# Kernel optimization log

Measured on AMD Instinct MI355X. Metric: run time of the kernel, lower is better.

Reference implementation:

```python
import jax, jax.numpy as jnp
import numpy as np

N_NODES = 50000
N_EDGES = 800000
D_IN = 96
D_OUT = 96


def setup_inputs() -> dict:
    key = jax.random.key(0)
    k1, k2, k3, k4 = jax.random.split(key, 4)
    feat = jax.random.normal(k1, (N_NODES, D_IN), dtype=jnp.float32)
    # xavier_normal-like init for weight, zeros bias (as in the torch module)
    std = (2.0 / (D_IN + D_OUT)) ** 0.5
    weight = jax.random.normal(k2, (D_IN, D_OUT), dtype=jnp.float32) * std
    bias = jnp.zeros((D_OUT,), dtype=jnp.float32)
    src = jax.random.randint(k3, (N_EDGES,), 0, N_NODES, dtype=jnp.int64)
    dst = jax.random.randint(k4, (N_EDGES,), 0, N_NODES, dtype=jnp.int64)
    return {"feat": feat, "weight": weight, "bias": bias, "src": src, "dst": dst}


def reference(feat, weight, bias, src, dst):
    N = feat.shape[0]
    ones = jnp.ones(src.shape[0], dtype=feat.dtype)
    out_deg = jax.ops.segment_sum(ones, src, num_segments=N)  # out-degree per node
    in_deg = jax.ops.segment_sum(ones, dst, num_segments=N)   # in-degree per node
    ci = jnp.clip(out_deg, 1.0, None) ** -0.5                 # src-side norm
    cj = jnp.clip(in_deg, 1.0, None) ** -0.5                  # dst-side norm
    # gather src features * ci, scatter-sum to dst, scale by cj
    msg = feat[src] * ci[src, None]                           # [E, D_IN]
    agg = jax.ops.segment_sum(msg, dst, num_segments=N) * cj[:, None]
    # DGL UDF reduce only updates nodes that receive messages; isolated
    # (zero in-degree) nodes keep their original features.
    h = jnp.where(in_deg[:, None] > 0, agg, feat)
    return jnp.matmul(h, weight) + bias
```

## Files before the change

### kernel.cpp

```cpp
#include <hip/hip_runtime.h>

#define N_NODES 50000
#define N_EDGES 800000
#define D 96
#define D4 (D / 4)

#define RL 12
#define HPAD 13

#define NB 196
#define ECAP 5120
#define SCAP 5120
#define HCCAP 3072
#define PA_BLOCKS 400
#define PA_CHUNK 2000
#define SB_BLOCKS 392
#define WPREP_TB 5

typedef __attribute__((ext_vector_type(8))) short short8;
typedef __attribute__((ext_vector_type(4))) float floatx4;

__device__ __forceinline__ short8 as_short8(uint4 u) { return *(short8*)&u; }

__device__ __forceinline__ unsigned bf16pack(float a, float b) {
    unsigned ua = __float_as_uint(a);
    unsigned ub = __float_as_uint(b);
    ua = (ua + 0x7FFFu + ((ua >> 16) & 1u)) >> 16;
    ub = (ub + 0x7FFFu + ((ub >> 16) & 1u)) & 0xFFFF0000u;
    return ua | ub;
}

__global__ void __launch_bounds__(1024) sortA_kernel(
        const int* __restrict__ src, const int* __restrict__ dst,
        unsigned* __restrict__ gcur,
        unsigned* __restrict__ ebuf, unsigned short* __restrict__ sbuf) {
    __shared__ unsigned raw[PA_CHUNK];
    __shared__ unsigned ord[PA_CHUNK];
    __shared__ unsigned short sord[PA_CHUNK];
    __shared__ unsigned hist[512];
    __shared__ unsigned sc[512], lstart[512], cur[512], gbase[512];
    int t = threadIdx.x;
    int e0 = blockIdx.x * PA_CHUNK;
    if (t < 512) hist[t] = 0;
    __syncthreads();
    for (int i = t; i < PA_CHUNK; i += 1024) {
        int s = src[e0 + i];
        int d = dst[e0 + i];
        raw[i] = ((unsigned)d << 16) | (unsigned)s;
        atomicAdd(&hist[d >> 8], 1u);
        atomicAdd(&hist[256 + (s >> 8)], 1u);
    }
    __syncthreads();
    if (t < 512) sc[t] = hist[t];
    __syncthreads();
    for (int o = 1; o < 256; o <<= 1) {
        unsigned v = 0;
        if (t < 512 && (t & 255) >= o) v = sc[t - o];
        __syncthreads();
        if (t < 512 && (t & 255) >= o) sc[t] += v;
        __syncthreads();
    }
    if (t < 512) {
        unsigned ls = sc[t] - hist[t];
        lstart[t] = ls;
        cur[t] = ls;
        if ((t & 255) < NB)
            gbase[t] = atomicAdd(&gcur[(t >> 8) * NB + (t & 255)], hist[t]);
    }
    __syncthreads();
    for (int i = t; i < PA_CHUNK; i += 1024) {
        unsigned r = raw[i];
        unsigned p = atomicAdd(&cur[r >> 24], 1u);
        ord[p] = r;
        unsigned s = r & 0xFFFFu;
        unsigned q = atomicAdd(&cur[256 + (s >> 8)], 1u);
        sord[q] = (unsigned short)s;
    }
    __syncthreads();
    for (int i = t; i < PA_CHUNK; i += 1024) {
        unsigned r = ord[i];
        unsigned bd = r >> 24;
        unsigned pos = gbase[bd] + ((unsigned)i - lstart[bd]);
        if (pos < ECAP) ebuf[bd * ECAP + pos] = r;
        unsigned s = sord[i];
        unsigned bs = 256 + (s >> 8);
        unsigned pos2 = gbase[bs] + ((unsigned)i - lstart[bs]);
        if (pos2 < SCAP) sbuf[(size_t)(bs - 256) * SCAP + pos2] = (unsigned short)s;
    }
}

__global__ void __launch_bounds__(1024) sortB_kernel(
        const unsigned* __restrict__ gcur, const unsigned* __restrict__ ebuf,
        const unsigned short* __restrict__ sbuf,
        const float4* __restrict__ feat4, const float* __restrict__ W,
        unsigned* __restrict__ WT32,
        int* __restrict__ deg_in, int* __restrict__ off,
        unsigned short* __restrict__ csr, uint4* __restrict__ sfeat) {
    int blk = blockIdx.x;
    if (blk >= SB_BLOCKS) {
        int t = (blk - SB_BLOCKS) * 1024 + threadIdx.x;
        if (t >= D * (D / 2)) return;
        int n = t / (D / 2);
        int j = t - n * (D / 2);
        float w0 = W[(2 * j) * D + n];
        float w1 = W[(2 * j + 1) * D + n];
        WT32[n * (D / 2) + j] = bf16pack(w0, w1);
        return;
    }
    __shared__ unsigned short csr_l[HCCAP];
    __shared__ unsigned dcount[128], dcur[128], scount[128];
    __shared__ unsigned wtot, tot_s;
    int b = blk >> 1;
    unsigned half = (unsigned)(blk & 1);
    int t = threadIdx.x;
    unsigned cntd = gcur[b];      if (cntd > ECAP) cntd = ECAP;
    unsigned cnts = gcur[NB + b]; if (cnts > SCAP) cnts = SCAP;
    if (t < 128) { dcount[t] = 0; scount[t] = 0; }
    __syncthreads();
    const unsigned* __restrict__ sg = ebuf + (size_t)b * ECAP;
    for (int i = t; i < (int)cntd; i += 1024) {
        unsigned loc = (sg[i] >> 16) & 255u;
        if ((loc >> 7) == half) atomicAdd(&dcount[loc & 127u], 1u);
    }
    const unsigned short* __restrict__ ss = sbuf + (size_t)b * SCAP;
    for (int i = t; i < (int)cnts; i += 1024) {
        unsigned loc = ss[i] & 255u;
        if ((loc >> 7) == half) atomicAdd(&scount[loc & 127u], 1u);
    }
    __syncthreads();
    unsigned pad = 0, incl = 0;
    if (t < 128) {
        pad = (dcount[t] + 7u) & ~7u;
        incl = pad;
        int lane = t & 63;
#pragma unroll
        for (int st = 1; st < 64; st <<= 1) {
            unsigned u = __shfl_up(incl, st, 64);
            if (lane >= st) incl += u;
        }
        if (t == 63) wtot = incl;
    }
    __syncthreads();
    if (t < 128) {
        if (t >= 64) incl += wtot;
        unsigned ex = incl - pad;
        dcur[t] = ex;
        if (t == 127) tot_s = incl;
        int n = b * 256 + (int)(half << 7) + t;
        if (n < N_NODES) {
            deg_in[n] = (int)dcount[t];
            off[n] = blk * HCCAP + (int)ex;
        }
    }
    __syncthreads();
    for (int i = t; i < (int)cntd; i += 1024) {
        unsigned r = sg[i];
        unsigned loc = (r >> 16) & 255u;
        if ((loc >> 7) == half) {
            unsigned p = atomicAdd(&dcur[loc & 127u], 1u);
            if (p < HCCAP) csr_l[p] = (unsigned short)(r & 0xFFFFu);
        }
    }
    __syncthreads();
    unsigned tot = tot_s;
    if (tot > HCCAP) tot = HCCAP;
    unsigned* __restrict__ og = (unsigned*)(csr + (size_t)blk * HCCAP);
    const unsigned* __restrict__ cl = (const unsigned*)csr_l;
    for (int i = t; i < (int)(tot >> 1); i += 1024) og[i] = cl[i];
    int base_n = b * 256 + (int)(half << 7);
    for (int r = t; r < 128 * RL; r += 1024) {
        int nl = r / RL;
        int lane = r - nl * RL;
        int n = base_n + nl;
        if (n < N_NODES) {
            float c = rsqrtf(fmaxf((float)scount[nl], 1.0f));
            float4 a = feat4[(size_t)n * D4 + lane * 2];
            float4 bb = feat4[(size_t)n * D4 + lane * 2 + 1];
            uint4 o;
            o.x = bf16pack(a.x * c, a.y * c);
            o.y = bf16pack(a.z * c, a.w * c);
            o.z = bf16pack(bb.x * c, bb.y * c);
            o.w = bf16pack(bb.z * c, bb.w * c);
            sfeat[(size_t)n * RL + lane] = o;
        }
    }
}

__global__ void __launch_bounds__(192) gather_mm_kernel(
        const float4* __restrict__ feat4, const uint4* __restrict__ sfeat,
        const int* __restrict__ deg_in, const int* __restrict__ off,
        const unsigned short* __restrict__ csr, const uint4* __restrict__ wt4,
        const float* __restrict__ bias, float* __restrict__ out) {
    __shared__ uint4 sh[16 * HPAD];
    int tid = threadIdx.x;
    {
        int g = tid / RL;
        int lane = tid - g * RL;
        int n = blockIdx.x * 16 + g;
        int deg = deg_in[n];
        uint4* __restrict__ hout = &sh[g * HPAD + lane];
        if (deg == 0) {
            float4 a = feat4[n * D4 + lane * 2];
            float4 b = feat4[n * D4 + lane * 2 + 1];
            uint4 o;
            o.x = bf16pack(a.x, a.y);
            o.y = bf16pack(a.z, a.w);
            o.z = bf16pack(b.x, b.y);
            o.w = bf16pack(b.z, b.w);
            *hout = o;
        } else {
            const unsigned short* __restrict__ bk = csr + off[n];
            const uint4* __restrict__ sf = sfeat + lane;
            float acc[8] = {};
#define ACC8(v)  { \
        acc[0] += __uint_as_float((v).x << 16); \
        acc[1] += __uint_as_float((v).x & 0xFFFF0000u); \
        acc[2] += __uint_as_float((v).y << 16); \
        acc[3] += __uint_as_float((v).y & 0xFFFF0000u); \
        acc[4] += __uint_as_float((v).z << 16); \
        acc[5] += __uint_as_float((v).z & 0xFFFF0000u); \
        acc[6] += __uint_as_float((v).w << 16); \
        acc[7] += __uint_as_float((v).w & 0xFFFF0000u); }
            int i = 0;
            int full16 = deg & ~15;
            for (; i < full16; i += 16) {
                uint4 ia = *(const uint4*)(bk + i);
                uint4 ib = *(const uint4*)(bk + i + 8);
                unsigned s0 = ia.x & 0xFFFFu, s1 = ia.x >> 16;
                unsigned s2 = ia.y & 0xFFFFu, s3 = ia.y >> 16;
                unsigned s4 = ia.z & 0xFFFFu, s5 = ia.z >> 16;
                unsigned s6 = ia.w & 0xFFFFu, s7 = ia.w >> 16;
                unsigned s8 = ib.x & 0xFFFFu, s9 = ib.x >> 16;
                unsigned sa = ib.y & 0xFFFFu, sb = ib.y >> 16;
                unsigned sx = ib.z & 0xFFFFu, sd = ib.z >> 16;
                unsigned se = ib.w & 0xFFFFu, sfi = ib.w >> 16;
                uint4 v0 = sf[(size_t)s0 * RL];
                uint4 v1 = sf[(size_t)s1 * RL];
                uint4 v2 = sf[(size_t)s2 * RL];
                uint4 v3 = sf[(size_t)s3 * RL];
                uint4 v4 = sf[(size_t)s4 * RL];
                uint4 v5 = sf[(size_t)s5 * RL];
                uint4 v6 = sf[(size_t)s6 * RL];
                uint4 v7 = sf[(size_t)s7 * RL];
                uint4 v8 = sf[(size_t)s8 * RL];
                uint4 v9 = sf[(size_t)s9 * RL];
                uint4 va = sf[(size_t)sa * RL];
                uint4 vb = sf[(size_t)sb * RL];
                uint4 vc = sf[(size_t)sx * RL];
                uint4 vd = sf[(size_t)sd * RL];
                uint4 ve = sf[(size_t)se * RL];
                uint4 vf = sf[(size_t)sfi * RL];
                ACC8(v0); ACC8(v1); ACC8(v2); ACC8(v3);
                ACC8(v4); ACC8(v5); ACC8(v6); ACC8(v7);
                ACC8(v8); ACC8(v9); ACC8(va); ACC8(vb);
                ACC8(vc); ACC8(vd); ACC8(ve); ACC8(vf);
            }
            int full8 = deg & ~7;
            for (; i < full8; i += 8) {
                uint4 idx = *(const uint4*)(bk + i);
                unsigned s0 = idx.x & 0xFFFFu, s1 = idx.x >> 16;
                unsigned s2 = idx.y & 0xFFFFu, s3 = idx.y >> 16;
                unsigned s4 = idx.z & 0xFFFFu, s5 = idx.z >> 16;
                unsigned s6 = idx.w & 0xFFFFu, s7 = idx.w >> 16;
                uint4 v0 = sf[(size_t)s0 * RL];
                uint4 v1 = sf[(size_t)s1 * RL];
                uint4 v2 = sf[(size_t)s2 * RL];
                uint4 v3 = sf[(size_t)s3 * RL];
                uint4 v4 = sf[(size_t)s4 * RL];
                uint4 v5 = sf[(size_t)s5 * RL];
                uint4 v6 = sf[(size_t)s6 * RL];
                uint4 v7 = sf[(size_t)s7 * RL];
                ACC8(v0); ACC8(v1); ACC8(v2); ACC8(v3);
                ACC8(v4); ACC8(v5); ACC8(v6); ACC8(v7);
            }
            for (; i < deg; ++i) {
                uint4 v = sf[(size_t)bk[i] * RL];
                ACC8(v);
            }
#undef ACC8
            float cj = rsqrtf((float)deg);
            uint4 o;
            o.x = bf16pack(acc[0] * cj, acc[1] * cj);
            o.y = bf16pack(acc[2] * cj, acc[3] * cj);
            o.z = bf16pack(acc[4] * cj, acc[5] * cj);
            o.w = bf16pack(acc[6] * cj, acc[7] * cj);
            *hout = o;
        }
    }
    __syncthreads();
    int wave = tid >> 6;
    int lane = tid & 63;
    int m = lane & 15, quad = lane >> 4;
    short8 a0 = as_short8(sh[m * HPAD + quad]);
    short8 a1 = as_short8(sh[m * HPAD + 4 + quad]);
    short8 a2 = as_short8(sh[m * HPAD + 8 + quad]);
    int row0 = blockIdx.x * 16;
    int r_out0 = row0 + quad * 4;
#pragma unroll
    for (int ct = wave * 2; ct < wave * 2 + 2; ++ct) {
        int n = ct * 16 + m;
        int wb = n * RL + quad;
        short8 b0 = as_short8(wt4[wb]);
        short8 b1 = as_short8(wt4[wb + 4]);
        short8 b2 = as_short8(wt4[wb + 8]);
        floatx4 c = {0.f, 0.f, 0.f, 0.f};
        c = __builtin_amdgcn_mfma_f32_16x16x32_bf16(a0, b0, c, 0, 0, 0);
        c = __builtin_amdgcn_mfma_f32_16x16x32_bf16(a1, b1, c, 0, 0, 0);
        c = __builtin_amdgcn_mfma_f32_16x16x32_bf16(a2, b2, c, 0, 0, 0);
        float bs = bias[n];
#pragma unroll
        for (int r = 0; r < 4; ++r)
            out[(size_t)(r_out0 + r) * D + n] = c[r] + bs;
    }
}

extern "C" void kernel_launch(void* const* d_in, const int* in_sizes, int n_in,
                              void* d_out, int out_size, void* d_ws, size_t ws_size,
                              hipStream_t stream) {
    const float* feat = (const float*)d_in[0];
    const float* W    = (const float*)d_in[1];
    const float* bias = (const float*)d_in[2];
    const int*   src  = (const int*)d_in[3];
    const int*   dst  = (const int*)d_in[4];

    unsigned*       gcur    = (unsigned*)d_ws;
    int*            deg_in  = (int*)(gcur + 2 * NB);
    int*            off     = deg_in + N_NODES;
    unsigned*       ebuf    = (unsigned*)(off + N_NODES);
    unsigned short* sbuf    = (unsigned short*)(ebuf + (size_t)NB * ECAP);
    unsigned short* csr     = sbuf + (size_t)NB * SCAP;
    uint4*          sfeat   = (uint4*)(csr + (size_t)SB_BLOCKS * HCCAP);
    unsigned*       WT32    = (unsigned*)(sfeat + (size_t)N_NODES * RL);

    hipMemsetAsync(gcur, 0, 2 * NB * sizeof(unsigned), stream);
    sortA_kernel<<<PA_BLOCKS, 1024, 0, stream>>>(src, dst, gcur, ebuf, sbuf);
    sortB_kernel<<<SB_BLOCKS + WPREP_TB, 1024, 0, stream>>>(
        gcur, ebuf, sbuf, (const float4*)feat, W, WT32, deg_in, off, csr, sfeat);
    gather_mm_kernel<<<N_NODES / 16, 192, 0, stream>>>(
        (const float4*)feat, sfeat, deg_in, off, csr, (const uint4*)WT32,
        bias, (float*)d_out);
}
```

Before: 139.8 us.

## Split neighbor gather across two thread teams and merge sortB halves

The gather kernel now runs 384 threads per 16-node tile. Two teams of 192 threads each take alternating 8-edge chunks of each node's neighbor list, and the partial sums are combined through shared memory before the MFMA transform. Each of the six waves then computes one 16-column output tile instead of two. sortB goes back to one block per 256-node bucket, staging the edge bucket in shared memory so the global buffer is read once instead of twice, at the cost of larger LDS use and fewer blocks. The aim is more memory-level parallelism for the latency-bound gather, in exchange for an extra shared-memory reduction and a barrier.

```diff
diff --git a/kernel.cpp b/kernel.cpp
--- a/kernel.cpp
+++ b/kernel.cpp
@@ -11,10 +11,9 @@
 #define NB 196
 #define ECAP 5120
 #define SCAP 5120
-#define HCCAP 3072
+#define CCAP 6144
 #define PA_BLOCKS 400
 #define PA_CHUNK 2000
-#define SB_BLOCKS 392
 #define WPREP_TB 5
 
 typedef __attribute__((ext_vector_type(8))) short short8;
@@ -97,39 +96,38 @@
         int* __restrict__ deg_in, int* __restrict__ off,
         unsigned short* __restrict__ csr, uint4* __restrict__ sfeat) {
     int blk = blockIdx.x;
-    if (blk >= SB_BLOCKS) {
-        int t = (blk - SB_BLOCKS) * 1024 + threadIdx.x;
-        if (t >= D * (D / 2)) return;
-        int n = t / (D / 2);
-        int j = t - n * (D / 2);
+    if (blk >= NB) {
+        int t2 = (blk - NB) * 1024 + threadIdx.x;
+        if (t2 >= D * (D / 2)) return;
+        int n = t2 / (D / 2);
+        int j = t2 - n * (D / 2);
         float w0 = W[(2 * j) * D + n];
         float w1 = W[(2 * j + 1) * D + n];
         WT32[n * (D / 2) + j] = bf16pack(w0, w1);
         return;
     }
-    __shared__ unsigned short csr_l[HCCAP];
-    __shared__ unsigned dcount[128], dcur[128], scount[128];
-    __shared__ unsigned wtot, tot_s;
-    int b = blk >> 1;
-    unsigned half = (unsigned)(blk & 1);
+    __shared__ unsigned eb[ECAP];
+    __shared__ unsigned short csr_l[CCAP];
+    __shared__ unsigned dcount[256], dcur[256], scount[256], wsum[4];
+    __shared__ unsigned tot_s;
+    int b = blk;
     int t = threadIdx.x;
     unsigned cntd = gcur[b];      if (cntd > ECAP) cntd = ECAP;
     unsigned cnts = gcur[NB + b]; if (cnts > SCAP) cnts = SCAP;
-    if (t < 128) { dcount[t] = 0; scount[t] = 0; }
+    if (t < 256) { dcount[t] = 0; scount[t] = 0; }
     __syncthreads();
     const unsigned* __restrict__ sg = ebuf + (size_t)b * ECAP;
     for (int i = t; i < (int)cntd; i += 1024) {
-        unsigned loc = (sg[i] >> 16) & 255u;
-        if ((loc >> 7) == half) atomicAdd(&dcount[loc & 127u], 1u);
+        unsigned r = sg[i];
+        eb[i] = r;
+        atomicAdd(&dcount[(r >> 16) & 255u], 1u);
     }
     const unsigned short* __restrict__ ss = sbuf + (size_t)b * SCAP;
-    for (int i = t; i < (int)cnts; i += 1024) {
-        unsigned loc = ss[i] & 255u;
-        if ((loc >> 7) == half) atomicAdd(&scount[loc & 127u], 1u);
-    }
+    for (int i = t; i < (int)cnts; i += 1024)
+        atomicAdd(&scount[ss[i] & 255u], 1u);
     __syncthreads();
     unsigned pad = 0, incl = 0;
-    if (t < 128) {
+    if (t < 256) {
         pad = (dcount[t] + 7u) & ~7u;
         incl = pad;
         int lane = t & 63;
@@ -138,40 +136,39 @@
             unsigned u = __shfl_up(incl, st, 64);
             if (lane >= st) incl += u;
         }
-        if (t == 63) wtot = incl;
-    }
-    __syncthreads();
-    if (t < 128) {
-        if (t >= 64) incl += wtot;
+        if (lane == 63) wsum[t >> 6] = incl;
+    }
+    __syncthreads();
+    if (t < 256) {
+        int w = t >> 6;
+        unsigned base = 0;
+        for (int k = 0; k < w; ++k) base += wsum[k];
+        incl += base;
         unsigned ex = incl - pad;
         dcur[t] = ex;
-        if (t == 127) tot_s = incl;
-        int n = b * 256 + (int)(half << 7) + t;
+        if (t == 255) tot_s = incl;
+        int n = b * 256 + t;
         if (n < N_NODES) {
             deg_in[n] = (int)dcount[t];
-            off[n] = blk * HCCAP + (int)ex;
+            off[n] = b * CCAP + (int)ex;
         }
     }
     __syncthreads();
     for (int i = t; i < (int)cntd; i += 1024) {
-        unsigned r = sg[i];
-        unsigned loc = (r >> 16) & 255u;
-        if ((loc >> 7) == half) {
-            unsigned p = atomicAdd(&dcur[loc & 127u], 1u);
-            if (p < HCCAP) csr_l[p] = (unsigned short)(r & 0xFFFFu);
-        }
+        unsigned r = eb[i];
+        unsigned p = atomicAdd(&dcur[(r >> 16) & 255u], 1u);
+        if (p < CCAP) csr_l[p] = (unsigned short)(r & 0xFFFFu);
     }
     __syncthreads();
     unsigned tot = tot_s;
-    if (tot > HCCAP) tot = HCCAP;
-    unsigned* __restrict__ og = (unsigned*)(csr + (size_t)blk * HCCAP);
+    if (tot > CCAP) tot = CCAP;
+    unsigned* __restrict__ og = (unsigned*)(csr + (size_t)b * CCAP);
     const unsigned* __restrict__ cl = (const unsigned*)csr_l;
     for (int i = t; i < (int)(tot >> 1); i += 1024) og[i] = cl[i];
-    int base_n = b * 256 + (int)(half << 7);
-    for (int r = t; r < 128 * RL; r += 1024) {
-        int nl = r / RL;
-        int lane = r - nl * RL;
-        int n = base_n + nl;
+    for (int r2 = t; r2 < 256 * RL; r2 += 1024) {
+        int nl = r2 / RL;
+        int lane = r2 - nl * RL;
+        int n = b * 256 + nl;
         if (n < N_NODES) {
             float c = rsqrtf(fmaxf((float)scount[nl], 1.0f));
             float4 a = feat4[(size_t)n * D4 + lane * 2];
@@ -186,32 +183,31 @@
     }
 }
 
-__global__ void __launch_bounds__(192) gather_mm_kernel(
+__global__ void __launch_bounds__(384) gather_mm_kernel(
         const float4* __restrict__ feat4, const uint4* __restrict__ sfeat,
         const int* __restrict__ deg_in, const int* __restrict__ off,
         const unsigned short* __restrict__ csr, const uint4* __restrict__ wt4,
         const float* __restrict__ bias, float* __restrict__ out) {
+    __shared__ float shp[16][D];
     __shared__ uint4 sh[16 * HPAD];
     int tid = threadIdx.x;
-    {
-        int g = tid / RL;
-        int lane = tid - g * RL;
-        int n = blockIdx.x * 16 + g;
-        int deg = deg_in[n];
-        uint4* __restrict__ hout = &sh[g * HPAD + lane];
-        if (deg == 0) {
-            float4 a = feat4[n * D4 + lane * 2];
-            float4 b = feat4[n * D4 + lane * 2 + 1];
-            uint4 o;
-            o.x = bf16pack(a.x, a.y);
-            o.y = bf16pack(a.z, a.w);
-            o.z = bf16pack(b.x, b.y);
-            o.w = bf16pack(b.z, b.w);
-            *hout = o;
-        } else {
-            const unsigned short* __restrict__ bk = csr + off[n];
-            const uint4* __restrict__ sf = sfeat + lane;
-            float acc[8] = {};
+    int team = (tid >= 192) ? 1 : 0;
+    int r = tid - team * 192;
+    int g = r / RL;
+    int lane = r - g * RL;
+    int n = blockIdx.x * 16 + g;
+    int deg = deg_in[n];
+    float acc[8] = {};
+    if (deg == 0) {
+        if (team == 0) {
+            float4 a = feat4[(size_t)n * D4 + lane * 2];
+            float4 b = feat4[(size_t)n * D4 + lane * 2 + 1];
+            acc[0] = a.x; acc[1] = a.y; acc[2] = a.z; acc[3] = a.w;
+            acc[4] = b.x; acc[5] = b.y; acc[6] = b.z; acc[7] = b.w;
+        }
+    } else {
+        const unsigned short* __restrict__ bk = csr + off[n];
+        const uint4* __restrict__ sf = sfeat + lane;
 #define ACC8(v)  { \
         acc[0] += __uint_as_float((v).x << 16); \
         acc[1] += __uint_as_float((v).x & 0xFFFF0000u); \
@@ -221,97 +217,75 @@
         acc[5] += __uint_as_float((v).z & 0xFFFF0000u); \
         acc[6] += __uint_as_float((v).w << 16); \
         acc[7] += __uint_as_float((v).w & 0xFFFF0000u); }
-            int i = 0;
-            int full16 = deg & ~15;
-            for (; i < full16; i += 16) {
-                uint4 ia = *(const uint4*)(bk + i);
-                uint4 ib = *(const uint4*)(bk + i + 8);
-                unsigned s0 = ia.x & 0xFFFFu, s1 = ia.x >> 16;
-                unsigned s2 = ia.y & 0xFFFFu, s3 = ia.y >> 16;
-                unsigned s4 = ia.z & 0xFFFFu, s5 = ia.z >> 16;
-                unsigned s6 = ia.w & 0xFFFFu, s7 = ia.w >> 16;
-                unsigned s8 = ib.x & 0xFFFFu, s9 = ib.x >> 16;
-                unsigned sa = ib.y & 0xFFFFu, sb = ib.y >> 16;
-                unsigned sx = ib.z & 0xFFFFu, sd = ib.z >> 16;
-                unsigned se = ib.w & 0xFFFFu, sfi = ib.w >> 16;
-                uint4 v0 = sf[(size_t)s0 * RL];
-                uint4 v1 = sf[(size_t)s1 * RL];
-                uint4 v2 = sf[(size_t)s2 * RL];
-                uint4 v3 = sf[(size_t)s3 * RL];
-                uint4 v4 = sf[(size_t)s4 * RL];
-                uint4 v5 = sf[(size_t)s5 * RL];
-                uint4 v6 = sf[(size_t)s6 * RL];
-                uint4 v7 = sf[(size_t)s7 * RL];
-                uint4 v8 = sf[(size_t)s8 * RL];
-                uint4 v9 = sf[(size_t)s9 * RL];
-                uint4 va = sf[(size_t)sa * RL];
-                uint4 vb = sf[(size_t)sb * RL];
-                uint4 vc = sf[(size_t)sx * RL];
-                uint4 vd = sf[(size_t)sd * RL];
-                uint4 ve = sf[(size_t)se * RL];
-                uint4 vf = sf[(size_t)sfi * RL];
-                ACC8(v0); ACC8(v1); ACC8(v2); ACC8(v3);
-                ACC8(v4); ACC8(v5); ACC8(v6); ACC8(v7);
-                ACC8(v8); ACC8(v9); ACC8(va); ACC8(vb);
-                ACC8(vc); ACC8(vd); ACC8(ve); ACC8(vf);
-            }
-            int full8 = deg & ~7;
-            for (; i < full8; i += 8) {
-                uint4 idx = *(const uint4*)(bk + i);
-                unsigned s0 = idx.x & 0xFFFFu, s1 = idx.x >> 16;
-                unsigned s2 = idx.y & 0xFFFFu, s3 = idx.y >> 16;
-                unsigned s4 = idx.z & 0xFFFFu, s5 = idx.z >> 16;
-                unsigned s6 = idx.w & 0xFFFFu, s7 = idx.w >> 16;
-                uint4 v0 = sf[(size_t)s0 * RL];
-                uint4 v1 = sf[(size_t)s1 * RL];
-                uint4 v2 = sf[(size_t)s2 * RL];
-                uint4 v3 = sf[(size_t)s3 * RL];
-                uint4 v4 = sf[(size_t)s4 * RL];
-                uint4 v5 = sf[(size_t)s5 * RL];
-                uint4 v6 = sf[(size_t)s6 * RL];
-                uint4 v7 = sf[(size_t)s7 * RL];
-                ACC8(v0); ACC8(v1); ACC8(v2); ACC8(v3);
-                ACC8(v4); ACC8(v5); ACC8(v6); ACC8(v7);
-            }
-            for (; i < deg; ++i) {
-                uint4 v = sf[(size_t)bk[i] * RL];
+        for (int i = team * 8; i + 8 <= deg; i += 16) {
+            uint4 idx = *(const uint4*)(bk + i);
+            unsigned s0 = idx.x & 0xFFFFu, s1 = idx.x >> 16;
+            unsigned s2 = idx.y & 0xFFFFu, s3 = idx.y >> 16;
+            unsigned s4 = idx.z & 0xFFFFu, s5 = idx.z >> 16;
+            unsigned s6 = idx.w & 0xFFFFu, s7 = idx.w >> 16;
+            uint4 v0 = sf[(size_t)s0 * RL];
+            uint4 v1 = sf[(size_t)s1 * RL];
+            uint4 v2 = sf[(size_t)s2 * RL];
+            uint4 v3 = sf[(size_t)s3 * RL];
+            uint4 v4 = sf[(size_t)s4 * RL];
+            uint4 v5 = sf[(size_t)s5 * RL];
+            uint4 v6 = sf[(size_t)s6 * RL];
+            uint4 v7 = sf[(size_t)s7 * RL];
+            ACC8(v0); ACC8(v1); ACC8(v2); ACC8(v3);
+            ACC8(v4); ACC8(v5); ACC8(v6); ACC8(v7);
+        }
+        int ts = deg & ~7;
+        if (((ts >> 3) & 1) == team) {
+            for (int j = ts; j < deg; ++j) {
+                uint4 v = sf[(size_t)bk[j] * RL];
                 ACC8(v);
             }
+        }
 #undef ACC8
-            float cj = rsqrtf((float)deg);
-            uint4 o;
-            o.x = bf16pack(acc[0] * cj, acc[1] * cj);
-            o.y = bf16pack(acc[2] * cj, acc[3] * cj);
-            o.z = bf16pack(acc[4] * cj, acc[5] * cj);
-            o.w = bf16pack(acc[6] * cj, acc[7] * cj);
-            *hout = o;
-        }
+    }
+    if (team == 0) {
+#pragma unroll
+        for (int j = 0; j < 8; ++j) shp[g][lane * 8 + j] = acc[j];
+    }
+    __syncthreads();
+    if (team == 1) {
+        float cj = (deg > 0) ? rsqrtf((float)deg) : 1.0f;
+        float s0 = (shp[g][lane * 8 + 0] + acc[0]) * cj;
+        float s1 = (shp[g][lane * 8 + 1] + acc[1]) * cj;
+        float s2 = (shp[g][lane * 8 + 2] + acc[2]) * cj;
+        float s3 = (shp[g][lane * 8 + 3] + acc[3]) * cj;
+        float s4 = (shp[g][lane * 8 + 4] + acc[4]) * cj;
+        float s5 = (shp[g][lane * 8 + 5] + acc[5]) * cj;
+        float s6 = (shp[g][lane * 8 + 6] + acc[6]) * cj;
+        float s7 = (shp[g][lane * 8 + 7] + acc[7]) * cj;
+        uint4 o;
+        o.x = bf16pack(s0, s1);
+        o.y = bf16pack(s2, s3);
+        o.z = bf16pack(s4, s5);
+        o.w = bf16pack(s6, s7);
+        sh[g * HPAD + lane] = o;
     }
     __syncthreads();
     int wave = tid >> 6;
-    int lane = tid & 63;
-    int m = lane & 15, quad = lane >> 4;
+    int lane64 = tid & 63;
+    int m = lane64 & 15, quad = lane64 >> 4;
     short8 a0 = as_short8(sh[m * HPAD + quad]);
     short8 a1 = as_short8(sh[m * HPAD + 4 + quad]);
     short8 a2 = as_short8(sh[m * HPAD + 8 + quad]);
-    int row0 = blockIdx.x * 16;
-    int r_out0 = row0 + quad * 4;
+    int nn = wave * 16 + m;
+    int wb = nn * RL + quad;
+    short8 b0 = as_short8(wt4[wb]);
+    short8 b1 = as_short8(wt4[wb + 4]);
+    short8 b2 = as_short8(wt4[wb + 8]);
+    floatx4 c = {0.f, 0.f, 0.f, 0.f};
+    c = __builtin_amdgcn_mfma_f32_16x16x32_bf16(a0, b0, c, 0, 0, 0);
+    c = __builtin_amdgcn_mfma_f32_16x16x32_bf16(a1, b1, c, 0, 0, 0);
+    c = __builtin_amdgcn_mfma_f32_16x16x32_bf16(a2, b2, c, 0, 0, 0);
+    float bs = bias[nn];
+    int r_out0 = blockIdx.x * 16 + quad * 4;
 #pragma unroll
-    for (int ct = wave * 2; ct < wave * 2 + 2; ++ct) {
-        int n = ct * 16 + m;
-        int wb = n * RL + quad;
-        short8 b0 = as_short8(wt4[wb]);
-        short8 b1 = as_short8(wt4[wb + 4]);
-        short8 b2 = as_short8(wt4[wb + 8]);
-        floatx4 c = {0.f, 0.f, 0.f, 0.f};
-        c = __builtin_amdgcn_mfma_f32_16x16x32_bf16(a0, b0, c, 0, 0, 0);
-        c = __builtin_amdgcn_mfma_f32_16x16x32_bf16(a1, b1, c, 0, 0, 0);
-        c = __builtin_amdgcn_mfma_f32_16x16x32_bf16(a2, b2, c, 0, 0, 0);
-        float bs = bias[n];
-#pragma unroll
-        for (int r = 0; r < 4; ++r)
-            out[(size_t)(r_out0 + r) * D + n] = c[r] + bs;
-    }
+    for (int rr = 0; rr < 4; ++rr)
+        out[(size_t)(r_out0 + rr) * D + nn] = c[rr] + bs;
 }
 
 extern "C" void kernel_launch(void* const* d_in, const int* in_sizes, int n_in,
@@ -329,14 +303,14 @@
     unsigned*       ebuf    = (unsigned*)(off + N_NODES);
     unsigned short* sbuf    = (unsigned short*)(ebuf + (size_t)NB * ECAP);
     unsigned short* csr     = sbuf + (size_t)NB * SCAP;
-    uint4*          sfeat   = (uint4*)(csr + (size_t)SB_BLOCKS * HCCAP);
+    uint4*          sfeat   = (uint4*)(csr + (size_t)NB * CCAP);
     unsigned*       WT32    = (unsigned*)(sfeat + (size_t)N_NODES * RL);
 
     hipMemsetAsync(gcur, 0, 2 * NB * sizeof(unsigned), stream);
     sortA_kernel<<<PA_BLOCKS, 1024, 0, stream>>>(src, dst, gcur, ebuf, sbuf);
-    sortB_kernel<<<SB_BLOCKS + WPREP_TB, 1024, 0, stream>>>(
+    sortB_kernel<<<NB + WPREP_TB, 1024, 0, stream>>>(
         gcur, ebuf, sbuf, (const float4*)feat, W, WT32, deg_in, off, csr, sfeat);
-    gather_mm_kernel<<<N_NODES / 16, 192, 0, stream>>>(
+    gather_mm_kernel<<<N_NODES / 16, 384, 0, stream>>>(
         (const float4*)feat, sfeat, deg_in, off, csr, (const uint4*)WT32,
         bias, (float*)d_out);
 }
```

Result: no change. 140.9 us (+0.8%).

## Fuse sort, CSR build and gather-matmul into one cooperative persistent kernel

Applied to the files above, without the earlier changes.

Merges the three kernel launches into a single cooperative kernel of 256 blocks that uses grid-wide syncs between phases: edge bucketing, per-bucket CSR/degree construction (one block per 256-node bucket instead of two half-buckets), and the gather plus MFMA matmul. The last phase loops over tiles, with five 192-thread groups per block. This removes launch gaps and the duplicated ebuf/sbuf scans. In exchange it runs with only 256 blocks, so latency hiding in the gather phase is lower, and it adds the cost of the grid syncs.

```diff
diff --git a/kernel.cpp b/kernel.cpp
--- a/kernel.cpp
+++ b/kernel.cpp
@@ -1,4 +1,7 @@
 #include <hip/hip_runtime.h>
+#include <hip/hip_cooperative_groups.h>
+
+namespace cg = cooperative_groups;
 
 #define N_NODES 50000
 #define N_EDGES 800000
@@ -11,11 +14,10 @@
 #define NB 196
 #define ECAP 5120
 #define SCAP 5120
-#define HCCAP 3072
-#define PA_BLOCKS 400
-#define PA_CHUNK 2000
-#define SB_BLOCKS 392
-#define WPREP_TB 5
+#define CCAP 6144
+#define PA_CHUNK 3125
+#define GRID_BLKS 256
+#define NT 3125
 
 typedef __attribute__((ext_vector_type(8))) short short8;
 typedef __attribute__((ext_vector_type(4))) float floatx4;
@@ -30,188 +32,207 @@
     return ua | ub;
 }
 
-__global__ void __launch_bounds__(1024) sortA_kernel(
+__global__ void __launch_bounds__(1024) fused_kernel(
         const int* __restrict__ src, const int* __restrict__ dst,
-        unsigned* __restrict__ gcur,
-        unsigned* __restrict__ ebuf, unsigned short* __restrict__ sbuf) {
-    __shared__ unsigned raw[PA_CHUNK];
-    __shared__ unsigned ord[PA_CHUNK];
-    __shared__ unsigned short sord[PA_CHUNK];
-    __shared__ unsigned hist[512];
-    __shared__ unsigned sc[512], lstart[512], cur[512], gbase[512];
+        const float4* __restrict__ feat4, const float* __restrict__ W,
+        const float* __restrict__ bias,
+        unsigned* __restrict__ gcur, unsigned* __restrict__ ebuf,
+        unsigned short* __restrict__ sbuf, unsigned short* __restrict__ csr,
+        uint4* __restrict__ sfeat, unsigned* __restrict__ WT32,
+        int* __restrict__ deg_in, int* __restrict__ off,
+        float* __restrict__ out) {
+    __shared__ __align__(16) char smem[41600];
+    __shared__ unsigned wsum8[8];
+    __shared__ unsigned tot_s;
+    cg::grid_group grid = cg::this_grid();
     int t = threadIdx.x;
-    int e0 = blockIdx.x * PA_CHUNK;
-    if (t < 512) hist[t] = 0;
-    __syncthreads();
-    for (int i = t; i < PA_CHUNK; i += 1024) {
-        int s = src[e0 + i];
-        int d = dst[e0 + i];
-        raw[i] = ((unsigned)d << 16) | (unsigned)s;
-        atomicAdd(&hist[d >> 8], 1u);
-        atomicAdd(&hist[256 + (s >> 8)], 1u);
+    int blk = blockIdx.x;
+
+    {
+        unsigned*       raw    = (unsigned*)(smem);
+        unsigned*       ord    = (unsigned*)(smem + 12544);
+        unsigned short* sord   = (unsigned short*)(smem + 25088);
+        unsigned*       hist   = (unsigned*)(smem + 31360);
+        unsigned*       lstart = (unsigned*)(smem + 35456);
+        unsigned*       cur    = (unsigned*)(smem + 37504);
+        unsigned*       gbase  = (unsigned*)(smem + 39552);
+        int e0 = blk * PA_CHUNK;
+        if (t < 512) hist[t] = 0;
+        __syncthreads();
+        for (int i = t; i < PA_CHUNK; i += 1024) {
+            int s = src[e0 + i];
+            int d = dst[e0 + i];
+            raw[i] = ((unsigned)d << 16) | (unsigned)s;
+            atomicAdd(&hist[d >> 8], 1u);
+            atomicAdd(&hist[256 + (s >> 8)], 1u);
+        }
+        __syncthreads();
+        unsigned h = 0, incl = 0;
+        if (t < 512) {
+            h = hist[t];
+            incl = h;
+            int lane = t & 63;
+#pragma unroll
+            for (int st = 1; st < 64; st <<= 1) {
+                unsigned u = __shfl_up(incl, st, 64);
+                if (lane >= st) incl += u;
+            }
+            if (lane == 63) wsum8[t >> 6] = incl;
+        }
+        __syncthreads();
+        if (t < 512) {
+            int w = t >> 6;
+            int h0 = (t >> 8) * 4;
+            unsigned base = 0;
+            for (int k = h0; k < w; ++k) base += wsum8[k];
+            incl += base;
+            unsigned ls = incl - h;
+            lstart[t] = ls;
+            cur[t] = ls;
+            if ((t & 255) < NB)
+                gbase[t] = atomicAdd(&gcur[(t >> 8) * NB + (t & 255)], h);
+        }
+        __syncthreads();
+        for (int i = t; i < PA_CHUNK; i += 1024) {
+            unsigned r = raw[i];
+            unsigned p = atomicAdd(&cur[r >> 24], 1u);
+            ord[p] = r;
+            unsigned s = r & 0xFFFFu;
+            unsigned q = atomicAdd(&cur[256 + (s >> 8)], 1u);
+            sord[q] = (unsigned short)s;
+        }
+        __syncthreads();
+        for (int i = t; i < PA_CHUNK; i += 1024) {
+            unsigned r = ord[i];
+            unsigned bd = r >> 24;
+            unsigned pos = gbase[bd] + ((unsigned)i - lstart[bd]);
+            if (pos < ECAP) ebuf[bd * ECAP + pos] = r;
+            unsigned s = sord[i];
+            unsigned bs = 256 + (s >> 8);
+            unsigned pos2 = gbase[bs] + ((unsigned)i - lstart[bs]);
+            if (pos2 < SCAP) sbuf[(size_t)(bs - 256) * SCAP + pos2] = (unsigned short)s;
+        }
     }
-    __syncthreads();
-    if (t < 512) sc[t] = hist[t];
-    __syncthreads();
-    for (int o = 1; o < 256; o <<= 1) {
-        unsigned v = 0;
-        if (t < 512 && (t & 255) >= o) v = sc[t - o];
-        __syncthreads();
-        if (t < 512 && (t & 255) >= o) sc[t] += v;
-        __syncthreads();
+    __threadfence();
+    grid.sync();
+
+    if (blk < NB) {
+        unsigned*       eb     = (unsigned*)(smem);
+        unsigned short* csr_l  = (unsigned short*)(smem + 20480);
+        unsigned*       dcount = (unsigned*)(smem + 32768);
+        unsigned*       dcur   = (unsigned*)(smem + 33792);
+        unsigned*       scount = (unsigned*)(smem + 34816);
+        int b = blk;
+        unsigned cntd = gcur[b];      if (cntd > ECAP) cntd = ECAP;
+        unsigned cnts = gcur[NB + b]; if (cnts > SCAP) cnts = SCAP;
+        if (t < 256) { dcount[t] = 0; scount[t] = 0; }
+        __syncthreads();
+        const unsigned* __restrict__ sg = ebuf + (size_t)b * ECAP;
+        for (int i = t; i < (int)cntd; i += 1024) {
+            unsigned r = sg[i];
+            eb[i] = r;
+            atomicAdd(&dcount[(r >> 16) & 255u], 1u);
+        }
+        const unsigned short* __restrict__ ss = sbuf + (size_t)b * SCAP;
+        for (int i = t; i < (int)cnts; i += 1024)
+            atomicAdd(&scount[ss[i] & 255u], 1u);
+        __syncthreads();
+        unsigned pad = 0, incl = 0;
+        if (t < 256) {
+            pad = (dcount[t] + 7u) & ~7u;
+            incl = pad;
+            int lane = t & 63;
+#pragma unroll
+            for (int st = 1; st < 64; st <<= 1) {
+                unsigned u = __shfl_up(incl, st, 64);
+                if (lane >= st) incl += u;
+            }
+            if (lane == 63) wsum8[t >> 6] = incl;
+        }
+        __syncthreads();
+        if (t < 256) {
+            int w = t >> 6;
+            unsigned base = 0;
+            for (int k = 0; k < w; ++k) base += wsum8[k];
+            incl += base;
+            unsigned ex = incl - pad;
+            dcur[t] = ex;
+            if (t == 255) tot_s = incl;
+            int n = b * 256 + t;
+            if (n < N_NODES) {
+                deg_in[n] = (int)dcount[t];
+                off[n] = b * CCAP + (int)ex;
+            }
+        }
+        __syncthreads();
+        for (int i = t; i < (int)cntd; i += 1024) {
+            unsigned r = eb[i];
+            unsigned p = atomicAdd(&dcur[(r >> 16) & 255u], 1u);
+            if (p < CCAP) csr_l[p] = (unsigned short)(r & 0xFFFFu);
+        }
+        __syncthreads();
+        unsigned tot = tot_s;
+        if (tot > CCAP) tot = CCAP;
+        unsigned* __restrict__ og = (unsigned*)(csr + (size_t)b * CCAP);
+        const unsigned* __restrict__ cl = (const unsigned*)csr_l;
+        for (int i = t; i < (int)(tot >> 1); i += 1024) og[i] = cl[i];
+        for (int r2 = t; r2 < 256 * RL; r2 += 1024) {
+            int nl = r2 / RL;
+            int lane = r2 - nl * RL;
+            int n = b * 256 + nl;
+            if (n < N_NODES) {
+                float c = rsqrtf(fmaxf((float)scount[nl], 1.0f));
+                float4 a = feat4[(size_t)n * D4 + lane * 2];
+                float4 bb = feat4[(size_t)n * D4 + lane * 2 + 1];
+                uint4 o;
+                o.x = bf16pack(a.x * c, a.y * c);
+                o.y = bf16pack(a.z * c, a.w * c);
+                o.z = bf16pack(bb.x * c, bb.y * c);
+                o.w = bf16pack(bb.z * c, bb.w * c);
+                sfeat[(size_t)n * RL + lane] = o;
+            }
+        }
+    } else {
+        int t2 = (blk - NB) * 1024 + t;
+        if (t2 < D * (D / 2)) {
+            int n = t2 / (D / 2);
+            int j = t2 - n * (D / 2);
+            float w0 = W[(2 * j) * D + n];
+            float w1 = W[(2 * j + 1) * D + n];
+            WT32[n * (D / 2) + j] = bf16pack(w0, w1);
+        }
     }
-    if (t < 512) {
-        unsigned ls = sc[t] - hist[t];
-        lstart[t] = ls;
-        cur[t] = ls;
-        if ((t & 255) < NB)
-            gbase[t] = atomicAdd(&gcur[(t >> 8) * NB + (t & 255)], hist[t]);
-    }
-    __syncthreads();
-    for (int i = t; i < PA_CHUNK; i += 1024) {
-        unsigned r = raw[i];
-        unsigned p = atomicAdd(&cur[r >> 24], 1u);
-        ord[p] = r;
-        unsigned s = r & 0xFFFFu;
-        unsigned q = atomicAdd(&cur[256 + (s >> 8)], 1u);
-        sord[q] = (unsigned short)s;
-    }
-    __syncthreads();
-    for (int i = t; i < PA_CHUNK; i += 1024) {
-        unsigned r = ord[i];
-        unsigned bd = r >> 24;
-        unsigned pos = gbase[bd] + ((unsigned)i - lstart[bd]);
-        if (pos < ECAP) ebuf[bd * ECAP + pos] = r;
-        unsigned s = sord[i];
-        unsigned bs = 256 + (s >> 8);
-        unsigned pos2 = gbase[bs] + ((unsigned)i - lstart[bs]);
-        if (pos2 < SCAP) sbuf[(size_t)(bs - 256) * SCAP + pos2] = (unsigned short)s;
-    }
-}
-
-__global__ void __launch_bounds__(1024) sortB_kernel(
-        const unsigned* __restrict__ gcur, const unsigned* __restrict__ ebuf,
-        const unsigned short* __restrict__ sbuf,
-        const float4* __restrict__ feat4, const float* __restrict__ W,
-        unsigned* __restrict__ WT32,
-        int* __restrict__ deg_in, int* __restrict__ off,
-        unsigned short* __restrict__ csr, uint4* __restrict__ sfeat) {
-    int blk = blockIdx.x;
-    if (blk >= SB_BLOCKS) {
-        int t = (blk - SB_BLOCKS) * 1024 + threadIdx.x;
-        if (t >= D * (D / 2)) return;
-        int n = t / (D / 2);
-        int j = t - n * (D / 2);
-        float w0 = W[(2 * j) * D + n];
-        float w1 = W[(2 * j + 1) * D + n];
-        WT32[n * (D / 2) + j] = bf16pack(w0, w1);
-        return;
-    }
-    __shared__ unsigned short csr_l[HCCAP];
-    __shared__ unsigned dcount[128], dcur[128], scount[128];
-    __shared__ unsigned wtot, tot_s;
-    int b = blk >> 1;
-    unsigned half = (unsigned)(blk & 1);
-    int t = threadIdx.x;
-    unsigned cntd = gcur[b];      if (cntd > ECAP) cntd = ECAP;
-    unsigned cnts = gcur[NB + b]; if (cnts > SCAP) cnts = SCAP;
-    if (t < 128) { dcount[t] = 0; scount[t] = 0; }
-    __syncthreads();
-    const unsigned* __restrict__ sg = ebuf + (size_t)b * ECAP;
-    for (int i = t; i < (int)cntd; i += 1024) {
-        unsigned loc = (sg[i] >> 16) & 255u;
-        if ((loc >> 7) == half) atomicAdd(&dcount[loc & 127u], 1u);
-    }
-    const unsigned short* __restrict__ ss = sbuf + (size_t)b * SCAP;
-    for (int i = t; i < (int)cnts; i += 1024) {
-        unsigned loc = ss[i] & 255u;
-        if ((loc >> 7) == half) atomicAdd(&scount[loc & 127u], 1u);
-    }
-    __syncthreads();
-    unsigned pad = 0, incl = 0;
-    if (t < 128) {
-        pad = (dcount[t] + 7u) & ~7u;
-        incl = pad;
-        int lane = t & 63;
-#pragma unroll
-        for (int st = 1; st < 64; st <<= 1) {
-            unsigned u = __shfl_up(incl, st, 64);
-            if (lane >= st) incl += u;
-        }
-        if (t == 63) wtot = incl;
-    }
-    __syncthreads();
-    if (t < 128) {
-        if (t >= 64) incl += wtot;
-        unsigned ex = incl - pad;
-        dcur[t] = ex;
-        if (t == 127) tot_s = incl;
-        int n = b * 256 + (int)(half << 7) + t;
-        if (n < N_NODES) {
-            deg_in[n] = (int)dcount[t];
-            off[n] = blk * HCCAP + (int)ex;
-        }
-    }
-    __syncthreads();
-    for (int i = t; i < (int)cntd; i += 1024) {
-        unsigned r = sg[i];
-        unsigned loc = (r >> 16) & 255u;
-        if ((loc >> 7) == half) {
-            unsigned p = atomicAdd(&dcur[loc & 127u], 1u);
-            if (p < HCCAP) csr_l[p] = (unsigned short)(r & 0xFFFFu);
-        }
-    }
-    __syncthreads();
-    unsigned tot = tot_s;
-    if (tot > HCCAP) tot = HCCAP;
-    unsigned* __restrict__ og = (unsigned*)(csr + (size_t)blk * HCCAP);
-    const unsigned* __restrict__ cl = (const unsigned*)csr_l;
-    for (int i = t; i < (int)(tot >> 1); i += 1024) og[i] = cl[i];
-    int base_n = b * 256 + (int)(half << 7);
-    for (int r = t; r < 128 * RL; r += 1024) {
-        int nl = r / RL;
-        int lane = r - nl * RL;
-        int n = base_n + nl;
-        if (n < N_NODES) {
-            float c = rsqrtf(fmaxf((float)scount[nl], 1.0f));
-            float4 a = feat4[(size_t)n * D4 + lane * 2];
-            float4 bb = feat4[(size_t)n * D4 + lane * 2 + 1];
-            uint4 o;
-            o.x = bf16pack(a.x * c, a.y * c);
-            o.y = bf16pack(a.z * c, a.w * c);
-            o.z = bf16pack(bb.x * c, bb.y * c);
-            o.w = bf16pack(bb.z * c, bb.w * c);
-            sfeat[(size_t)n * RL + lane] = o;
-        }
-    }
-}
-
-__global__ void __launch_bounds__(192) gather_mm_kernel(
-        const float4* __restrict__ feat4, const uint4* __restrict__ sfeat,
-        const int* __restrict__ deg_in, const int* __restrict__ off,
-        const unsigned short* __restrict__ csr, const uint4* __restrict__ wt4,
-        const float* __restrict__ bias, float* __restrict__ out) {
-    __shared__ uint4 sh[16 * HPAD];
-    int tid = threadIdx.x;
+    __threadfence();
+    grid.sync();
+
     {
-        int g = tid / RL;
-        int lane = tid - g * RL;
-        int n = blockIdx.x * 16 + g;
-        int deg = deg_in[n];
-        uint4* __restrict__ hout = &sh[g * HPAD + lane];
-        if (deg == 0) {
-            float4 a = feat4[n * D4 + lane * 2];
-            float4 b = feat4[n * D4 + lane * 2 + 1];
-            uint4 o;
-            o.x = bf16pack(a.x, a.y);
-            o.y = bf16pack(a.z, a.w);
-            o.z = bf16pack(b.x, b.y);
-            o.w = bf16pack(b.z, b.w);
-            *hout = o;
-        } else {
-            const unsigned short* __restrict__ bk = csr + off[n];
-            const uint4* __restrict__ sf = sfeat + lane;
-            float acc[8] = {};
+        const uint4* __restrict__ wt4 = (const uint4*)WT32;
+        int grp = t / 192;
+        int r = t - grp * 192;
+        uint4* shg = (uint4*)(smem + grp * 3328);
+        for (int j = 0; j < 3; ++j) {
+            int tile = j * 1280 + blk * 5 + grp;
+            bool active = (t < 960) && (tile < NT);
+            int deg = 0;
+            if (active) {
+                int g = r / RL;
+                int lane = r - g * RL;
+                int n = tile * 16 + g;
+                deg = deg_in[n];
+                uint4* __restrict__ hout = &shg[g * HPAD + lane];
+                if (deg == 0) {
+                    float4 a = feat4[(size_t)n * D4 + lane * 2];
+                    float4 b = feat4[(size_t)n * D4 + lane * 2 + 1];
+                    uint4 o;
+                    o.x = bf16pack(a.x, a.y);
+                    o.y = bf16pack(a.z, a.w);
+                    o.z = bf16pack(b.x, b.y);
+                    o.w = bf16pack(b.z, b.w);
+                    *hout = o;
+                } else {
+                    const unsigned short* __restrict__ bk = csr + off[n];
+                    const uint4* __restrict__ sf = sfeat + lane;
+                    float acc[8] = {};
 #define ACC8(v)  { \
         acc[0] += __uint_as_float((v).x << 16); \
         acc[1] += __uint_as_float((v).x & 0xFFFF0000u); \
@@ -221,122 +242,128 @@
         acc[5] += __uint_as_float((v).z & 0xFFFF0000u); \
         acc[6] += __uint_as_float((v).w << 16); \
         acc[7] += __uint_as_float((v).w & 0xFFFF0000u); }
-            int i = 0;
-            int full16 = deg & ~15;
-            for (; i < full16; i += 16) {
-                uint4 ia = *(const uint4*)(bk + i);
-                uint4 ib = *(const uint4*)(bk + i + 8);
-                unsigned s0 = ia.x & 0xFFFFu, s1 = ia.x >> 16;
-                unsigned s2 = ia.y & 0xFFFFu, s3 = ia.y >> 16;
-                unsigned s4 = ia.z & 0xFFFFu, s5 = ia.z >> 16;
-                unsigned s6 = ia.w & 0xFFFFu, s7 = ia.w >> 16;
-                unsigned s8 = ib.x & 0xFFFFu, s9 = ib.x >> 16;
-                unsigned sa = ib.y & 0xFFFFu, sb = ib.y >> 16;
-                unsigned sx = ib.z & 0xFFFFu, sd = ib.z >> 16;
-                unsigned se = ib.w & 0xFFFFu, sfi = ib.w >> 16;
-                uint4 v0 = sf[(size_t)s0 * RL];
-                uint4 v1 = sf[(size_t)s1 * RL];
-                uint4 v2 = sf[(size_t)s2 * RL];
-                uint4 v3 = sf[(size_t)s3 * RL];
-                uint4 v4 = sf[(size_t)s4 * RL];
-                uint4 v5 = sf[(size_t)s5 * RL];
-                uint4 v6 = sf[(size_t)s6 * RL];
-                uint4 v7 = sf[(size_t)s7 * RL];
-                uint4 v8 = sf[(size_t)s8 * RL];
-                uint4 v9 = sf[(size_t)s9 * RL];
-                uint4 va = sf[(size_t)sa * RL];
-                uint4 vb = sf[(size_t)sb * RL];
-                uint4 vc = sf[(size_t)sx * RL];
-                uint4 vd = sf[(size_t)sd * RL];
-                uint4 ve = sf[(size_t)se * RL];
-                uint4 vf = sf[(size_t)sfi * RL];
-                ACC8(v0); ACC8(v1); ACC8(v2); ACC8(v3);
-                ACC8(v4); ACC8(v5); ACC8(v6); ACC8(v7);
-                ACC8(v8); ACC8(v9); ACC8(va); ACC8(vb);
-                ACC8(vc); ACC8(vd); ACC8(ve); ACC8(vf);
-            }
-            int full8 = deg & ~7;
-            for (; i < full8; i += 8) {
-                uint4 idx = *(const uint4*)(bk + i);
-                unsigned s0 = idx.x & 0xFFFFu, s1 = idx.x >> 16;
-                unsigned s2 = idx.y & 0xFFFFu, s3 = idx.y >> 16;
-                unsigned s4 = idx.z & 0xFFFFu, s5 = idx.z >> 16;
-                unsigned s6 = idx.w & 0xFFFFu, s7 = idx.w >> 16;
-                uint4 v0 = sf[(size_t)s0 * RL];
-                uint4 v1 = sf[(size_t)s1 * RL];
-                uint4 v2 = sf[(size_t)s2 * RL];
-                uint4 v3 = sf[(size_t)s3 * RL];
-                uint4 v4 = sf[(size_t)s4 * RL];
-                uint4 v5 = sf[(size_t)s5 * RL];
-                uint4 v6 = sf[(size_t)s6 * RL];
-                uint4 v7 = sf[(size_t)s7 * RL];
-                ACC8(v0); ACC8(v1); ACC8(v2); ACC8(v3);
-                ACC8(v4); ACC8(v5); ACC8(v6); ACC8(v7);
-            }
-            for (; i < deg; ++i) {
-                uint4 v = sf[(size_t)bk[i] * RL];
-                ACC8(v);
-            }
+                    int i = 0;
+                    int full16 = deg & ~15;
+                    for (; i < full16; i += 16) {
+                        uint4 ia = *(const uint4*)(bk + i);
+                        uint4 ib = *(const uint4*)(bk + i + 8);
+                        unsigned s0 = ia.x & 0xFFFFu, s1 = ia.x >> 16;
+                        unsigned s2 = ia.y & 0xFFFFu, s3 = ia.y >> 16;
+                        unsigned s4 = ia.z & 0xFFFFu, s5 = ia.z >> 16;
+                        unsigned s6 = ia.w & 0xFFFFu, s7 = ia.w >> 16;
+                        unsigned s8 = ib.x & 0xFFFFu, s9 = ib.x >> 16;
+                        unsigned sa = ib.y & 0xFFFFu, sb = ib.y >> 16;
+                        unsigned sx = ib.z & 0xFFFFu, sd = ib.z >> 16;
+                        unsigned se = ib.w & 0xFFFFu, sfi = ib.w >> 16;
+                        uint4 v0 = sf[(size_t)s0 * RL];
+                        uint4 v1 = sf[(size_t)s1 * RL];
+                        uint4 v2 = sf[(size_t)s2 * RL];
+                        uint4 v3 = sf[(size_t)s3 * RL];
+                        uint4 v4 = sf[(size_t)s4 * RL];
+                        uint4 v5 = sf[(size_t)s5 * RL];
+                        uint4 v6 = sf[(size_t)s6 * RL];
+                        uint4 v7 = sf[(size_t)s7 * RL];
+                        uint4 v8 = sf[(size_t)s8 * RL];
+                        uint4 v9 = sf[(size_t)s9 * RL];
+                        uint4 va = sf[(size_t)sa * RL];
+                        uint4 vb = sf[(size_t)sb * RL];
+                        uint4 vc = sf[(size_t)sx * RL];
+                        uint4 vd = sf[(size_t)sd * RL];
+                        uint4 ve = sf[(size_t)se * RL];
+                        uint4 vf = sf[(size_t)sfi * RL];
+                        ACC8(v0); ACC8(v1); ACC8(v2); ACC8(v3);
+                        ACC8(v4); ACC8(v5); ACC8(v6); ACC8(v7);
+                        ACC8(v8); ACC8(v9); ACC8(va); ACC8(vb);
+                        ACC8(vc); ACC8(vd); ACC8(ve); ACC8(vf);
+                    }
+                    int full8 = deg & ~7;
+                    for (; i < full8; i += 8) {
+                        uint4 idx = *(const uint4*)(bk + i);
+                        unsigned s0 = idx.x & 0xFFFFu, s1 = idx.x >> 16;
+                        unsigned s2 = idx.y & 0xFFFFu, s3 = idx.y >> 16;
+                        unsigned s4 = idx.z & 0xFFFFu, s5 = idx.z >> 16;
+                        unsigned s6 = idx.w & 0xFFFFu, s7 = idx.w >> 16;
+                        uint4 v0 = sf[(size_t)s0 * RL];
+                        uint4 v1 = sf[(size_t)s1 * RL];
+                        uint4 v2 = sf[(size_t)s2 * RL];
+                        uint4 v3 = sf[(size_t)s3 * RL];
+                        uint4 v4 = sf[(size_t)s4 * RL];
+                        uint4 v5 = sf[(size_t)s5 * RL];
+                        uint4 v6 = sf[(size_t)s6 * RL];
+                        uint4 v7 = sf[(size_t)s7 * RL];
+                        ACC8(v0); ACC8(v1); ACC8(v2); ACC8(v3);
+                        ACC8(v4); ACC8(v5); ACC8(v6); ACC8(v7);
+                    }
+                    for (; i < deg; ++i) {
+                        uint4 v = sf[(size_t)bk[i] * RL];
+                        ACC8(v);
+                    }
 #undef ACC8
-            float cj = rsqrtf((float)deg);
-            uint4 o;
-            o.x = bf16pack(acc[0] * cj, acc[1] * cj);
-            o.y = bf16pack(acc[2] * cj, acc[3] * cj);
-            o.z = bf16pack(acc[4] * cj, acc[5] * cj);
-            o.w = bf16pack(acc[6] * cj, acc[7] * cj);
-            *hout = o;
-        }
-    }
-    __syncthreads();
-    int wave = tid >> 6;
-    int lane = tid & 63;
-    int m = lane & 15, quad = lane >> 4;
-    short8 a0 = as_short8(sh[m * HPAD + quad]);
-    short8 a1 = as_short8(sh[m * HPAD + 4 + quad]);
-    short8 a2 = as_short8(sh[m * HPAD + 8 + quad]);
-    int row0 = blockIdx.x * 16;
-    int r_out0 = row0 + quad * 4;
+                    float cj = rsqrtf((float)deg);
+                    uint4 o;
+                    o.x = bf16pack(acc[0] * cj, acc[1] * cj);
+                    o.y = bf16pack(acc[2] * cj, acc[3] * cj);
+                    o.z = bf16pack(acc[4] * cj, acc[5] * cj);
+                    o.w = bf16pack(acc[6] * cj, acc[7] * cj);
+                    *hout = o;
+                }
+            }
+            __syncthreads();
+            if (active) {
+                int wave = r >> 6;
+                int lane64 = r & 63;
+                int m = lane64 & 15, quad = lane64 >> 4;
+                short8 a0 = as_short8(shg[m * HPAD + quad]);
+                short8 a1 = as_short8(shg[m * HPAD + 4 + quad]);
+                short8 a2 = as_short8(shg[m * HPAD + 8 + quad]);
+                int r_out0 = tile * 16 + quad * 4;
 #pragma unroll
-    for (int ct = wave * 2; ct < wave * 2 + 2; ++ct) {
-        int n = ct * 16 + m;
-        int wb = n * RL + quad;
-        short8 b0 = as_short8(wt4[wb]);
-        short8 b1 = as_short8(wt4[wb + 4]);
-        short8 b2 = as_short8(wt4[wb + 8]);
-        floatx4 c = {0.f, 0.f, 0.f, 0.f};
-        c = __builtin_amdgcn_mfma_f32_16x16x32_bf16(a0, b0, c, 0, 0, 0);
-        c = __builtin_amdgcn_mfma_f32_16x16x32_bf16(a1, b1, c, 0, 0, 0);
-        c = __builtin_amdgcn_mfma_f32_16x16x32_bf16(a2, b2, c, 0, 0, 0);
-        float bs = bias[n];
+                for (int ct = wave * 2; ct < wave * 2 + 2; ++ct) {
+                    int nn = ct * 16 + m;
+                    int wb = nn * RL + quad;
+                    short8 b0 = as_short8(wt4[wb]);
+                    short8 b1 = as_short8(wt4[wb + 4]);
+                    short8 b2 = as_short8(wt4[wb + 8]);
+                    floatx4 c = {0.f, 0.f, 0.f, 0.f};
+                    c = __builtin_amdgcn_mfma_f32_16x16x32_bf16(a0, b0, c, 0, 0, 0);
+                    c = __builtin_amdgcn_mfma_f32_16x16x32_bf16(a1, b1, c, 0, 0, 0);
+                    c = __builtin_amdgcn_mfma_f32_16x16x32_bf16(a2, b2, c, 0, 0, 0);
+                    float bs = bias[nn];
 #pragma unroll
-        for (int r = 0; r < 4; ++r)
-            out[(size_t)(r_out0 + r) * D + n] = c[r] + bs;
+                    for (int rr = 0; rr < 4; ++rr)
+                        out[(size_t)(r_out0 + rr) * D + nn] = c[rr] + bs;
+                }
+            }
+            __syncthreads();
+        }
     }
 }
 
 extern "C" void kernel_launch(void* const* d_in, const int* in_sizes, int n_in,
                               void* d_out, int out_size, void* d_ws, size_t ws_size,
                               hipStream_t stream) {
-    const float* feat = (const float*)d_in[0];
-    const float* W    = (const float*)d_in[1];
-    const float* bias = (const float*)d_in[2];
-    const int*   src  = (const int*)d_in[3];
-    const int*   dst  = (const int*)d_in[4];
-
-    unsigned*       gcur    = (unsigned*)d_ws;
-    int*            deg_in  = (int*)(gcur + 2 * NB);
-    int*            off     = deg_in + N_NODES;
-    unsigned*       ebuf    = (unsigned*)(off + N_NODES);
-    unsigned short* sbuf    = (unsigned short*)(ebuf + (size_t)NB * ECAP);
-    unsigned short* csr     = sbuf + (size_t)NB * SCAP;
-    uint4*          sfeat   = (uint4*)(csr + (size_t)SB_BLOCKS * HCCAP);
-    unsigned*       WT32    = (unsigned*)(sfeat + (size_t)N_NODES * RL);
+    const int*    src   = (const int*)d_in[3];
+    const int*    dst   = (const int*)d_in[4];
+    const float4* feat4 = (const float4*)d_in[0];
+    const float*  W     = (const float*)d_in[1];
+    const float*  bias  = (const float*)d_in[2];
+
+    unsigned*       gcur   = (unsigned*)d_ws;
+    int*            deg_in = (int*)(gcur + 2 * NB);
+    int*            off    = deg_in + N_NODES;
+    unsigned*       ebuf   = (unsigned*)(off + N_NODES);
+    unsigned short* sbuf   = (unsigned short*)(ebuf + (size_t)NB * ECAP);
+    unsigned short* csr    = sbuf + (size_t)NB * SCAP;
+    uint4*          sfeat  = (uint4*)(csr + (size_t)NB * CCAP);
+    unsigned*       WT32   = (unsigned*)(sfeat + (size_t)N_NODES * RL);
+    float*          out    = (float*)d_out;
 
     hipMemsetAsync(gcur, 0, 2 * NB * sizeof(unsigned), stream);
-    sortA_kernel<<<PA_BLOCKS, 1024, 0, stream>>>(src, dst, gcur, ebuf, sbuf);
-    sortB_kernel<<<SB_BLOCKS + WPREP_TB, 1024, 0, stream>>>(
-        gcur, ebuf, sbuf, (const float4*)feat, W, WT32, deg_in, off, csr, sfeat);
-    gather_mm_kernel<<<N_NODES / 16, 192, 0, stream>>>(
-        (const float4*)feat, sfeat, deg_in, off, csr, (const uint4*)WT32,
-        bias, (float*)d_out);
+    void* args[] = {
+        (void*)&src, (void*)&dst, (void*)&feat4, (void*)&W, (void*)&bias,
+        (void*)&gcur, (void*)&ebuf, (void*)&sbuf, (void*)&csr,
+        (void*)&sfeat, (void*)&WT32, (void*)&deg_in, (void*)&off, (void*)&out
+    };
+    hipLaunchCooperativeKernel((const void*)fused_kernel, dim3(GRID_BLKS),
+                               dim3(1024), args, 0, stream);
 }
```

New measurement: 400.1 us. 2.86x slower.
